# Performance work log

Measured on AMD Instinct MI355X. Metric: run time of the kernel, lower is better.

Reference implementation:

```python
import jax, jax.numpy as jnp
import numpy as np

N_NODES = 100000
N_EDGES = 640000
D_IN = 128
HIDDEN = 256
OUT = 256
NUM_GRAPHS = 256


def setup_inputs() -> dict:
    key = jax.random.key(0)
    ks = jax.random.split(key, 8)
    x = jax.random.normal(ks[0], (N_NODES, D_IN), dtype=jnp.float32)
    edge_index = jax.random.randint(ks[1], (2, N_EDGES), 0, N_NODES, dtype=jnp.int64)
    batch = jnp.sort(jax.random.randint(ks[2], (N_NODES,), 0, NUM_GRAPHS, dtype=jnp.int64))
    s1 = 1.0 / np.sqrt(D_IN)
    s2 = 1.0 / np.sqrt(HIDDEN)
    W1_l = jax.random.normal(ks[3], (D_IN, HIDDEN), dtype=jnp.float32) * s1
    W1_r = jax.random.normal(ks[4], (D_IN, HIDDEN), dtype=jnp.float32) * s1
    b1 = jnp.zeros((HIDDEN,), dtype=jnp.float32)
    W2_l = jax.random.normal(ks[5], (HIDDEN, OUT), dtype=jnp.float32) * s2
    W2_r = jax.random.normal(ks[6], (HIDDEN, OUT), dtype=jnp.float32) * s2
    b2 = jnp.zeros((OUT,), dtype=jnp.float32)
    return {"x": x, "edge_index": edge_index, "batch": batch,
            "W1_l": W1_l, "b1": b1, "W1_r": W1_r,
            "W2_l": W2_l, "b2": b2, "W2_r": W2_r}


def _sage_conv(x, src, dst, W_l, b_l, W_r):
    # PyG SAGEConv, aggr='mean': lin_l(mean_{j in N(i)} x_j) + lin_r(x_i)
    n = x.shape[0]
    msgs = x[src]                                              # [E, d] gather
    agg = jax.ops.segment_sum(msgs, dst, num_segments=n)       # [N, d] scatter-add
    cnt = jax.ops.segment_sum(jnp.ones((src.shape[0],), x.dtype), dst, num_segments=n)
    mean = agg / jnp.maximum(cnt, 1.0)[:, None]
    return mean @ W_l + b_l + x @ W_r


def reference(x, edge_index, batch, W1_l, b1, W1_r, W2_l, b2, W2_r):
    src, dst = edge_index[0], edge_index[1]
    h = jax.nn.relu(_sage_conv(x, src, dst, W1_l, b1, W1_r))
    h = _sage_conv(h, src, dst, W2_l, b2, W2_r)
    # global_add_pool: segment sum over per-node graph ids
    return jax.ops.segment_sum(h, batch, num_segments=NUM_GRAPHS)  # [G, OUT]
```

## Files before the change

kernel.cpp:

```cpp
#include <hip/hip_runtime.h>

#define NN 100000
#define NE 640000
#define DIN 128
#define DH 256
#define DOUT 256
#define NG 256
#define NB1 ((NN + 255) / 256)

#define PECH 157
#define CPE (4 * PECH)
#define PEB ((NE + CPE - 1) / CPE)
#define GSP 8

#define PNB 1024
#define CHN2 ((NN + PNB - 1) / PNB)

#define BCH 4096
#define BNB ((NE + BCH - 1) / BCH)

#define XCB (NN * DIN / 8 / 256)
#define CTB ((NE + 255) / 256)

typedef __bf16 bf16_t;
typedef __bf16 bf16x8 __attribute__((ext_vector_type(8)));
typedef __bf16 bf16x2 __attribute__((ext_vector_type(2)));
typedef float f32x4 __attribute__((ext_vector_type(4)));
typedef float f32v2 __attribute__((ext_vector_type(2)));

#if __has_builtin(__builtin_amdgcn_cvt_pk_fp8_f32) && __has_builtin(__builtin_amdgcn_cvt_pk_f32_fp8)
#define USE_HW_FP8 1
#else
#define USE_HW_FP8 0
#endif

#if !USE_HW_FP8
__device__ __forceinline__ unsigned f32_to_fp8_1(float f) {
  unsigned sg = (__float_as_uint(f) >> 31) << 7;
  float af = fabsf(f);
  unsigned body;
  if (af < 0.015625f) {
    body = (unsigned)(int)rintf(af * 512.0f);
  } else {
    unsigned bits = __float_as_uint(af);
    unsigned rb = bits + 0x7FFFFu + ((bits >> 20) & 1u);
    unsigned e = rb >> 23;
    body = ((e - 120u) << 3) | ((rb >> 20) & 7u);
  }
  return (sg | body) & 0xffu;
}
__device__ __forceinline__ float fp8_to_f32_1(unsigned b) {
  unsigned s = b >> 7, e = (b >> 3) & 15u, m = b & 7u;
  float v = (e == 0) ? (float)m * 0.001953125f
                     : __uint_as_float(((e + 120u) << 23) | (m << 20));
  return s ? -v : v;
}
#endif

__device__ __forceinline__ unsigned pack4_fp8(float v0, float v1, float v2, float v3) {
#if USE_HW_FP8
  int u = __builtin_amdgcn_cvt_pk_fp8_f32(v0, v1, 0, false);
  u = __builtin_amdgcn_cvt_pk_fp8_f32(v2, v3, u, true);
  return (unsigned)u;
#else
  return f32_to_fp8_1(v0) | (f32_to_fp8_1(v1) << 8) |
         (f32_to_fp8_1(v2) << 16) | (f32_to_fp8_1(v3) << 24);
#endif
}

__device__ __forceinline__ void unpack4_fp8(unsigned v, float* o) {
#if USE_HW_FP8
  f32v2 a = __builtin_amdgcn_cvt_pk_f32_fp8((int)v, false);
  f32v2 b = __builtin_amdgcn_cvt_pk_f32_fp8((int)v, true);
  o[0] = a[0]; o[1] = a[1]; o[2] = b[0]; o[3] = b[1];
#else
  o[0] = fp8_to_f32_1(v & 0xffu);         o[1] = fp8_to_f32_1((v >> 8) & 0xffu);
  o[2] = fp8_to_f32_1((v >> 16) & 0xffu); o[3] = fp8_to_f32_1(v >> 24);
#endif
}

__device__ __forceinline__ void unpack2_fp8(unsigned v, float* o) {
#if USE_HW_FP8
  f32v2 a = __builtin_amdgcn_cvt_pk_f32_fp8((int)v, false);
  o[0] = a[0]; o[1] = a[1];
#else
  o[0] = fp8_to_f32_1(v & 0xffu); o[1] = fp8_to_f32_1((v >> 8) & 0xffu);
#endif
}

__global__ void k_pre(const float* __restrict__ x, const int* __restrict__ dst,
                      const float* __restrict__ Wl, const float* __restrict__ Wr,
                      unsigned char* __restrict__ xf8, int* __restrict__ cnt,
                      bf16_t* __restrict__ Bp) {
  int b = blockIdx.x;
  if (b < XCB) {
    size_t i = ((size_t)b * 256 + threadIdx.x) * 8;
    float4 a = *(const float4*)(x + i), c = *(const float4*)(x + i + 4);
    uint2 p;
    p.x = pack4_fp8(a.x, a.y, a.z, a.w);
    p.y = pack4_fp8(c.x, c.y, c.z, c.w);
    *(uint2*)(xf8 + i) = p;
  } else if (b < XCB + CTB) {
    int e = (b - XCB) * 256 + threadIdx.x;
    if (e < NE) atomicAdd(&cnt[dst[e]], 1);
  } else {
    int t = (b - XCB - CTB) * 256 + threadIdx.x;
    if (t < 8192) {
      int lane = t & 63, nt = (t >> 6) & 15, kc = t >> 10;
      int n = nt * 16 + (lane & 15);
      int k0 = kc * 32 + (lane >> 4) * 8;
      bf16_t* o = Bp + ((size_t)(kc * 16 + nt) * 64 + lane) * 8;
      for (int j = 0; j < 8; ++j) {
        int k = k0 + j;
        float v = (k < 128) ? Wl[k * 256 + n] : Wr[(k - 128) * 256 + n];
        o[j] = (bf16_t)v;
      }
    }
  }
}

__global__ void k_scan1(const int* __restrict__ cnt, int* __restrict__ rpl,
                        int* __restrict__ part) {
  __shared__ int s[256];
  int t = threadIdx.x, i = blockIdx.x * 256 + t;
  int v = (i < NN) ? cnt[i] : 0;
  s[t] = v; __syncthreads();
#pragma unroll
  for (int off = 1; off < 256; off <<= 1) {
    int u = (t >= off) ? s[t - off] : 0;
    __syncthreads();
    s[t] += u;
    __syncthreads();
  }
  if (i < NN) rpl[i] = s[t] - v;
  if (t == 255) part[blockIdx.x] = s[255];
}

__global__ void k_scan2(int* __restrict__ part) {
  __shared__ int s[512];
  int t = threadIdx.x;
  int v = (t < NB1) ? part[t] : 0;
  s[t] = v; __syncthreads();
#pragma unroll
  for (int off = 1; off < 512; off <<= 1) {
    int u = (t >= off) ? s[t - off] : 0;
    __syncthreads();
    s[t] += u;
    __syncthreads();
  }
  if (t < NB1) part[t] = s[t] - v;
}

__global__ void k_finish(const int* __restrict__ rpl, const int* __restrict__ part,
                         const int* __restrict__ batch, int* __restrict__ rowptr,
                         int* __restrict__ gstart, unsigned* __restrict__ wg) {
  int n = blockIdx.x * 256 + threadIdx.x;
  if (n >= NN) return;
  int r0 = rpl[n] + part[n >> 8];
  int r1 = (n + 1 < NN) ? (rpl[n + 1] + part[(n + 1) >> 8]) : NE;
  rowptr[n] = r0;
  if (n == 0) rowptr[NN] = NE;
  int b = batch[n];
  int prev = (n == 0) ? -1 : batch[n - 1];
  for (int g = prev + 1; g <= b; ++g) gstart[g] = n;
  if (n == NN - 1) {
    for (int g = b + 1; g <= NG; ++g) gstart[g] = NN;
  }
  unsigned val = ((unsigned)b << 16) | (unsigned)(r1 - r0);
  for (int e = r0; e < r1; ++e) wg[e] = val;
}

__global__ void k_bucket(const int* __restrict__ src, const int* __restrict__ dst,
                         const int* __restrict__ rowptr, int* __restrict__ fill,
                         int* __restrict__ col) {
  int cls = blockIdx.x & 7;
  int cb = blockIdx.x >> 3;
  int e0 = cb * BCH;
  int e1 = (e0 + BCH < NE) ? e0 + BCH : NE;
  for (int e = e0 + threadIdx.x; e < e1; e += 256) {
    int d = dst[e];
    if (((d >> 4) & 7) == cls) {
      int p = rowptr[d] + atomicAdd(&fill[d], 1);
      col[p] = src[e];
    }
  }
}

__launch_bounds__(256, 4)
__global__ void k_gemm1(const unsigned char* __restrict__ xf8,
                        const int* __restrict__ rowptr, const int* __restrict__ col,
                        const float* __restrict__ b1,
                        const bf16_t* __restrict__ Bp, unsigned char* __restrict__ hf8) {
  __shared__ unsigned char smem[64 * 512];
  int n0 = blockIdx.x * 64;
  int tid = threadIdx.x;
  int wave = tid >> 6, lane = tid & 63;
  {
    int base = __builtin_amdgcn_readfirstlane(n0 + wave * 16);
    int nb1 = base + 16; if (nb1 > NN) nb1 = NN;
    if (base < NN) {
      int e = rowptr[base];
      int eTot = rowptr[nb1];
      int n = base;
      int estart = e;
      int eend = rowptr[n + 1];
      float a0 = 0.f, a1 = 0.f;
#define GFLUSH()                                                               \
      do {                                                                     \
        float r = (eend > estart)                                              \
                    ? __builtin_amdgcn_rcpf((float)(eend - estart)) : 0.f;     \
        int row = n - n0;                                                      \
        unsigned sw = (row & 7) << 4;                                          \
        bf16x2 mv; mv[0] = (bf16_t)(a0 * r); mv[1] = (bf16_t)(a1 * r);         \
        *(bf16x2*)(smem + row * 512 + (((unsigned)(lane * 4)) ^ sw)) = mv;     \
        a0 = 0.f; a1 = 0.f;                                                    \
        estart = eend; ++n;                                                    \
        if (n < nb1) eend = rowptr[n + 1];                                     \
      } while (0)
      while (e + 8 <= eTot) {
        unsigned v[8];
#pragma unroll
        for (int i = 0; i < 8; ++i) {
          int s = col[e + i];
          v[i] = *(const unsigned short*)(xf8 + (size_t)s * DIN + lane * 2);
        }
#pragma unroll
        for (int i = 0; i < 8; ++i) {
          while (e + i >= eend) GFLUSH();
          float o[2]; unpack2_fp8(v[i], o);
          a0 += o[0]; a1 += o[1];
        }
        e += 8;
      }
      while (e < eTot) {
        int s = col[e];
        unsigned v = *(const unsigned short*)(xf8 + (size_t)s * DIN + lane * 2);
        while (e >= eend) GFLUSH();
        float o[2]; unpack2_fp8(v, o);
        a0 += o[0]; a1 += o[1];
        ++e;
      }
      while (n < nb1) GFLUSH();
#undef GFLUSH
    }
#pragma unroll
    for (int i = 0; i < 16; ++i) {
      int node = base + i;
      int row = wave * 16 + i;
      unsigned sw = (row & 7) << 4;
      unsigned v = 0;
      if (node < NN) v = *(const unsigned short*)(xf8 + (size_t)node * DIN + lane * 2);
      float o[2]; unpack2_fp8(v, o);
      bf16x2 xv; xv[0] = (bf16_t)o[0]; xv[1] = (bf16_t)o[1];
      *(bf16x2*)(smem + row * 512 + ((unsigned)(256 + lane * 4) ^ sw)) = xv;
    }
  }
  __syncthreads();
  int lhi = lane >> 4, llo = lane & 15;
  f32x4 acc[4][4] = {};
  const bf16x8* bptr = (const bf16x8*)Bp;
#pragma unroll
  for (int kc = 0; kc < 8; ++kc) {
    bf16x8 a[4], b[4];
#pragma unroll
    for (int mi = 0; mi < 4; ++mi) {
      int row = mi * 16 + llo;
      unsigned cb = ((unsigned)((kc * 32 + lhi * 8) * 2)) ^ ((row & 7) << 4);
      a[mi] = *(const bf16x8*)(smem + row * 512 + cb);
    }
#pragma unroll
    for (int ni = 0; ni < 4; ++ni)
      b[ni] = bptr[(kc * 16 + wave * 4 + ni) * 64 + lane];
#pragma unroll
    for (int mi = 0; mi < 4; ++mi)
#pragma unroll
      for (int ni = 0; ni < 4; ++ni)
        acc[mi][ni] = __builtin_amdgcn_mfma_f32_16x16x32_bf16(a[mi], b[ni], acc[mi][ni], 0, 0, 0);
  }
  float bias[4];
#pragma unroll
  for (int ni = 0; ni < 4; ++ni) bias[ni] = b1[wave * 64 + ni * 16 + llo];
#pragma unroll
  for (int mi = 0; mi < 4; ++mi)
#pragma unroll
    for (int j = 0; j < 4; ++j) {
      int node = n0 + mi * 16 + lhi * 4 + j;
      if (node < NN) {
        float v0 = fmaxf(acc[mi][0][j] + bias[0], 0.f);
        float v1 = fmaxf(acc[mi][1][j] + bias[1], 0.f);
        float v2 = fmaxf(acc[mi][2][j] + bias[2], 0.f);
        float v3 = fmaxf(acc[mi][3][j] + bias[3], 0.f);
        unsigned u = pack4_fp8(v0, v1, v2, v3);
        *(unsigned*)(hf8 + (size_t)node * 256 + wave * 64 + llo * 4) = u;
      }
    }
}

__global__ void k_pool(const int* __restrict__ col, const unsigned* __restrict__ wg,
                       const int* __restrict__ batch, const unsigned char* __restrict__ hf8,
                       float* __restrict__ Y1, float* __restrict__ Y2) {
  __shared__ float gbuf[GSP][256];
  int tid = threadIdx.x;
  int wv = tid >> 6, lane = tid & 63;
  int dmb = ((lane >> 4) << 6) | (lane & 15);
  float acc[4] = {0.f, 0.f, 0.f, 0.f};
  int curg = -1;
  if (blockIdx.x < PEB) {
    int c0 = blockIdx.x * CPE;
    int c1 = (c0 + CPE < NE) ? c0 + CPE : NE;
    if (c0 >= c1) return;
    int gmin = (int)(wg[c0] >> 16), gmax = (int)(wg[c1 - 1] >> 16);
    bool ldsok = (gmax - gmin) < GSP;
    for (int i = tid; i < GSP * 256; i += 256) (&gbuf[0][0])[i] = 0.f;
    __syncthreads();
    int e0 = __builtin_amdgcn_readfirstlane(c0 + wv * PECH);
    int e1 = e0 + PECH; if (e1 > c1) e1 = c1;
#define EFLUSH() do { if (curg >= 0) {                                        \
    if (ldsok) { float* gp = gbuf[curg - gmin];                               \
      atomicAdd(gp + (dmb | 0),  acc[0]); atomicAdd(gp + (dmb | 16), acc[1]); \
      atomicAdd(gp + (dmb | 32), acc[2]); atomicAdd(gp + (dmb | 48), acc[3]); \
    } else { float* yp = Y1 + (size_t)curg * 256;                             \
      unsafeAtomicAdd(yp + (dmb | 0),  acc[0]);                               \
      unsafeAtomicAdd(yp + (dmb | 16), acc[1]);                               \
      unsafeAtomicAdd(yp + (dmb | 32), acc[2]);                               \
      unsafeAtomicAdd(yp + (dmb | 48), acc[3]); }                             \
    acc[0] = acc[1] = acc[2] = acc[3] = 0.f; } } while (0)
    if (e0 < e1) {
      int e = e0;
      for (; e + 16 <= e1; e += 16) {
        unsigned wvv[16]; unsigned hv[16];
#pragma unroll
        for (int i = 0; i < 16; ++i) {
          int c = col[e + i];
          wvv[i] = wg[e + i];
          hv[i] = *(const unsigned*)(hf8 + (size_t)c * 256 + lane * 4);
        }
#pragma unroll
        for (int i = 0; i < 16; ++i) {
          int g = (int)(wvv[i] >> 16);
          if (g != curg) { EFLUSH(); curg = g; }
          float w = __builtin_amdgcn_rcpf((float)(wvv[i] & 0xffffu));
          float o[4]; unpack4_fp8(hv[i], o);
          acc[0] += w * o[0]; acc[1] += w * o[1];
          acc[2] += w * o[2]; acc[3] += w * o[3];
        }
      }
      for (; e < e1; ++e) {
        int c = col[e]; unsigned wv2 = wg[e];
        unsigned hvv = *(const unsigned*)(hf8 + (size_t)c * 256 + lane * 4);
        int g = (int)(wv2 >> 16);
        if (g != curg) { EFLUSH(); curg = g; }
        float w = __builtin_amdgcn_rcpf((float)(wv2 & 0xffffu));
        float o[4]; unpack4_fp8(hvv, o);
        acc[0] += w * o[0]; acc[1] += w * o[1];
        acc[2] += w * o[2]; acc[3] += w * o[3];
      }
      EFLUSH();
    }
#undef EFLUSH
    __syncthreads();
    if (ldsok) {
      int ng = gmax - gmin + 1;
      for (int gi = 0; gi < ng; ++gi)
        unsafeAtomicAdd(&Y1[(size_t)(gmin + gi) * 256 + tid], gbuf[gi][tid]);
    }
  } else {
    int nb = blockIdx.x - PEB;
    int n0 = nb * CHN2;
    int n1 = (n0 + CHN2 < NN) ? n0 + CHN2 : NN;
    if (n0 >= n1) return;
    int gmin = batch[n0], gmax = batch[n1 - 1];
    bool ldsok = (gmax - gmin) < GSP;
    for (int i = tid; i < GSP * 256; i += 256) (&gbuf[0][0])[i] = 0.f;
    __syncthreads();
    const int per = (CHN2 + 3) >> 2;
    int a0 = n0 + wv * per;
    int a1 = a0 + per; if (a1 > n1) a1 = n1;
#define NFLUSH() do { if (curg >= 0) {                                        \
    if (ldsok) { float* gp = gbuf[curg - gmin];                               \
      atomicAdd(gp + (dmb | 0),  acc[0]); atomicAdd(gp + (dmb | 16), acc[1]); \
      atomicAdd(gp + (dmb | 32), acc[2]); atomicAdd(gp + (dmb | 48), acc[3]); \
    } else { float* yp = Y2 + (size_t)curg * 256;                             \
      unsafeAtomicAdd(yp + (dmb | 0),  acc[0]);                               \
      unsafeAtomicAdd(yp + (dmb | 16), acc[1]);                               \
      unsafeAtomicAdd(yp + (dmb | 32), acc[2]);                               \
      unsafeAtomicAdd(yp + (dmb | 48), acc[3]); }                             \
    acc[0] = acc[1] = acc[2] = acc[3] = 0.f; } } while (0)
    for (int n = a0; n < a1; ++n) {
      int g = batch[n];
      if (g != curg) { NFLUSH(); curg = g; }
      unsigned v = *(const unsigned*)(hf8 + (size_t)n * 256 + lane * 4);
      float o[4]; unpack4_fp8(v, o);
      acc[0] += o[0]; acc[1] += o[1]; acc[2] += o[2]; acc[3] += o[3];
    }
    NFLUSH();
#undef NFLUSH
    __syncthreads();
    if (ldsok) {
      int ng = gmax - gmin + 1;
      for (int gi = 0; gi < ng; ++gi)
        unsafeAtomicAdd(&Y2[(size_t)(gmin + gi) * 256 + tid], gbuf[gi][tid]);
    }
  }
}

__global__ void k_out2(const float* __restrict__ Y1, const float* __restrict__ Y2,
                       const float* __restrict__ W2l, const float* __restrict__ W2r,
                       const float* __restrict__ b2, const int* __restrict__ gstart,
                       float* __restrict__ out) {
  __shared__ float ys[128];
  int g = blockIdx.x, ks = blockIdx.y, t = threadIdx.x;
  const float* Ysrc = (ks < 2) ? Y1 : Y2;
  const float* Wsrc = (ks < 2) ? W2l : W2r;
  int kbase = (ks & 1) * 128;
  if (t < 128) ys[t] = Ysrc[(size_t)g * 256 + kbase + t];
  __syncthreads();
  float s = 0.f;
  const float* wp = Wsrc + (size_t)kbase * 256 + t;
#pragma unroll 8
  for (int k = 0; k < 128; ++k) s += ys[k] * wp[(size_t)k * 256];
  if (ks == 0) {
    float cntf = (float)(gstart[g + 1] - gstart[g]);
    s += b2[t] * cntf;
  }
  unsafeAtomicAdd(&out[(size_t)g * 256 + t], s);
}

extern "C" void kernel_launch(void* const* d_in, const int* in_sizes, int n_in,
                              void* d_out, int out_size, void* d_ws, size_t ws_size,
                              hipStream_t stream) {
  const float* x   = (const float*)d_in[0];
  const int*   ei  = (const int*)d_in[1];
  const int*   bat = (const int*)d_in[2];
  const float* W1l = (const float*)d_in[3];
  const float* b1  = (const float*)d_in[4];
  const float* W1r = (const float*)d_in[5];
  const float* W2l = (const float*)d_in[6];
  const float* b2  = (const float*)d_in[7];
  const float* W2r = (const float*)d_in[8];
  const int* src = ei;
  const int* dst = ei + NE;

  char* ws = (char*)d_ws;
  size_t off = 0;
  int* cnt     = (int*)(ws + off); off += ((size_t)NN * 4 + 255) & ~(size_t)255;
  int* rpl     = (int*)(ws + off); off += ((size_t)(NN + 1) * 4 + 255) & ~(size_t)255;
  int* rowptr  = (int*)(ws + off); off += ((size_t)(NN + 1) * 4 + 255) & ~(size_t)255;
  int* part    = (int*)(ws + off); off += 512 * 4;
  int* fill    = (int*)(ws + off); off += ((size_t)NN * 4 + 255) & ~(size_t)255;
  int* gstart  = (int*)(ws + off); off += ((size_t)(NG + 1) * 4 + 255) & ~(size_t)255;
  int* col     = (int*)(ws + off); off += (size_t)NE * 4;
  unsigned* wg = (unsigned*)(ws + off); off += (size_t)NE * 4;
  bf16_t* Bp1  = (bf16_t*)(ws + off); off += (size_t)256 * 256 * 2;
  float* Y1    = (float*)(ws + off); off += (size_t)NG * 256 * 4;
  float* Y2    = (float*)(ws + off); off += (size_t)NG * 256 * 4;
  unsigned char* xf8 = (unsigned char*)(ws + off); off += (size_t)NN * DIN;
  unsigned char* hf8 = (unsigned char*)(ws + off); off += (size_t)NN * DH;

  hipMemsetAsync(cnt, 0, (size_t)NN * 4, stream);
  hipMemsetAsync(fill, 0, (size_t)NN * 4, stream);
  hipMemsetAsync(Y1, 0, (size_t)NG * 256 * 4 * 2, stream);
  hipMemsetAsync(d_out, 0, (size_t)out_size * 4, stream);
  k_pre<<<XCB + CTB + 32, 256, 0, stream>>>(x, dst, W1l, W1r, xf8, cnt, Bp1);
  k_scan1<<<NB1, 256, 0, stream>>>(cnt, rpl, part);
  k_scan2<<<1, 512, 0, stream>>>(part);
  k_finish<<<NB1, 256, 0, stream>>>(rpl, part, bat, rowptr, gstart, wg);
  k_bucket<<<BNB * 8, 256, 0, stream>>>(src, dst, rowptr, fill, col);
  k_gemm1<<<(NN + 63) / 64, 256, 0, stream>>>(xf8, rowptr, col, b1, Bp1, hf8);
  k_pool<<<PEB + PNB, 256, 0, stream>>>(col, wg, bat, hf8, Y1, Y2);
  k_out2<<<dim3(NG, 4), 256, 0, stream>>>(Y1, Y2, W2l, W2r, b2, gstart, (float*)d_out);
}
```

Baseline: 185.4 us.

## Double-buffer neighbor gathers and cache rowptr in lanes for gemm1 aggregation

The mean-aggregation prologue of k_gemm1 now loads the wave's 17 rowptr entries once into lanes and reads them back with readlane, replacing repeated scalar loads. The gather loop is double-buffered: the next batch of 8 neighbor rows is issued before the current batch is accumulated, hiding gather latency. Tail handling merges into the main loop with clamped indices, and launch bounds rise to 5 waves per SIMD, which may constrain registers and cause spills alongside the extra buffer.

```diff
diff --git a/kernel.cpp b/kernel.cpp
--- a/kernel.cpp
+++ b/kernel.cpp
@@ -186,7 +186,7 @@
   }
 }
 
-__launch_bounds__(256, 4)
+__launch_bounds__(256, 5)
 __global__ void k_gemm1(const unsigned char* __restrict__ xf8,
                         const int* __restrict__ rowptr, const int* __restrict__ col,
                         const float* __restrict__ b1,
@@ -199,48 +199,67 @@
     int base = __builtin_amdgcn_readfirstlane(n0 + wave * 16);
     int nb1 = base + 16; if (nb1 > NN) nb1 = NN;
     if (base < NN) {
-      int e = rowptr[base];
-      int eTot = rowptr[nb1];
+      int rpidx = base + (lane < 16 ? lane : 16);
+      if (rpidx > NN) rpidx = NN;
+      int rpv = rowptr[rpidx];
+      int span = nb1 - base;
+      int e0 = __builtin_amdgcn_readlane(rpv, 0);
+      int eTot = __builtin_amdgcn_readlane(rpv, span);
       int n = base;
-      int estart = e;
-      int eend = rowptr[n + 1];
+      int estart = e0;
+      int eend = __builtin_amdgcn_readlane(rpv, 1);
       float a0 = 0.f, a1 = 0.f;
 #define GFLUSH()                                                               \
       do {                                                                     \
-        float r = (eend > estart)                                              \
-                    ? __builtin_amdgcn_rcpf((float)(eend - estart)) : 0.f;     \
-        int row = n - n0;                                                      \
-        unsigned sw = (row & 7) << 4;                                          \
-        bf16x2 mv; mv[0] = (bf16_t)(a0 * r); mv[1] = (bf16_t)(a1 * r);         \
-        *(bf16x2*)(smem + row * 512 + (((unsigned)(lane * 4)) ^ sw)) = mv;     \
+        float r_ = (eend > estart)                                             \
+                     ? __builtin_amdgcn_rcpf((float)(eend - estart)) : 0.f;    \
+        int row_ = n - n0;                                                     \
+        unsigned sw_ = (row_ & 7) << 4;                                        \
+        bf16x2 mv_; mv_[0] = (bf16_t)(a0 * r_); mv_[1] = (bf16_t)(a1 * r_);    \
+        *(bf16x2*)(smem + row_ * 512 + (((unsigned)(lane * 4)) ^ sw_)) = mv_;  \
         a0 = 0.f; a1 = 0.f;                                                    \
         estart = eend; ++n;                                                    \
-        if (n < nb1) eend = rowptr[n + 1];                                     \
+        if (n < nb1) eend = __builtin_amdgcn_readlane(rpv, n - base + 1);      \
       } while (0)
-      while (e + 8 <= eTot) {
-        unsigned v[8];
-#pragma unroll
-        for (int i = 0; i < 8; ++i) {
-          int s = col[e + i];
-          v[i] = *(const unsigned short*)(xf8 + (size_t)s * DIN + lane * 2);
+#define LOADB(dst, off)                                                        \
+      do {                                                                     \
+        _Pragma("unroll")                                                      \
+        for (int i_ = 0; i_ < 8; ++i_) {                                       \
+          int ee_ = (off) + i_; if (ee_ > eTot - 1) ee_ = eTot - 1;            \
+          int s_ = col[ee_];                                                   \
+          dst[i_] = *(const unsigned short*)(xf8 + (size_t)s_ * DIN + lane * 2); \
+        }                                                                      \
+      } while (0)
+#define PROCB(vv, bb)                                                          \
+      do {                                                                     \
+        int ebase_ = e0 + (bb) * 8;                                            \
+        _Pragma("unroll")                                                      \
+        for (int i_ = 0; i_ < 8; ++i_) {                                       \
+          if (ebase_ + i_ < eTot) {                                            \
+            while (ebase_ + i_ >= eend) GFLUSH();                              \
+            float o_[2]; unpack2_fp8(vv[i_], o_);                              \
+            a0 += o_[0]; a1 += o_[1];                                          \
+          }                                                                    \
+        }                                                                      \
+      } while (0)
+      int nE = eTot - e0;
+      if (nE > 0) {
+        unsigned va[8], vb[8];
+        int nB = (nE + 7) >> 3;
+        LOADB(va, e0);
+        int b = 0;
+        for (;;) {
+          if (b + 1 < nB) LOADB(vb, e0 + (b + 1) * 8);
+          PROCB(va, b);
+          ++b; if (b >= nB) break;
+          if (b + 1 < nB) LOADB(va, e0 + (b + 1) * 8);
+          PROCB(vb, b);
+          ++b; if (b >= nB) break;
         }
-#pragma unroll
-        for (int i = 0; i < 8; ++i) {
-          while (e + i >= eend) GFLUSH();
-          float o[2]; unpack2_fp8(v[i], o);
-          a0 += o[0]; a1 += o[1];
-        }
-        e += 8;
-      }
-      while (e < eTot) {
-        int s = col[e];
-        unsigned v = *(const unsigned short*)(xf8 + (size_t)s * DIN + lane * 2);
-        while (e >= eend) GFLUSH();
-        float o[2]; unpack2_fp8(v, o);
-        a0 += o[0]; a1 += o[1];
-        ++e;
       }
       while (n < nb1) GFLUSH();
+#undef PROCB
+#undef LOADB
 #undef GFLUSH
     }
 #pragma unroll
```

Result: slower. 189.2 us (+2.1%).
